# Optimization experiments

Measured on AMD Instinct MI355X. Metric: run time of the kernel, lower is better.

## Reference

```python
import jax, jax.numpy as jnp
import numpy as np

X = 2048      # hidden units per layer
Z = 4         # number of hidden layers
IN = 512      # input_dim
OUT = 256     # output_dim
B = 64        # batch
T = 128       # time steps
KEEP = 0.7    # Bernoulli keep prob y
RES = [0, 0, 1, 2]  # residual_in (first two unused by the branch structure)
NFUN = 5      # number of candidate transfer functions


def setup_inputs() -> dict:
    key = jax.random.key(0)
    ks = jax.random.split(key, 12)
    f32 = jnp.float32
    x = jax.random.normal(ks[0], (B, T, IN), f32)
    W_in = jax.random.normal(ks[1], (X, IN), f32) * jax.random.bernoulli(ks[2], KEEP, (X, IN)).astype(f32)
    b_in = jax.random.normal(ks[3], (X,), f32)
    W_h = jax.random.normal(ks[4], (Z, X, 2 * X), f32)
    # lateral inhibition block: hidden layer 1, second-half columns, zero diagonal
    lat = jax.random.normal(ks[5], (X, X), f32) * (1.0 - jnp.eye(X, dtype=f32))
    W_h = W_h.at[1, :, X:].set(lat)
    W_h = W_h * jax.random.bernoulli(ks[6], KEEP, (Z, X, 2 * X)).astype(f32)
    b_h = jax.random.normal(ks[7], (Z, X), f32)
    W_out = jax.random.normal(ks[8], (OUT, X), f32) * jax.random.bernoulli(ks[9], KEEP, (OUT, X)).astype(f32)
    b_out = jax.random.normal(ks[10], (OUT,), f32)
    act_ids = jax.random.randint(ks[11], (Z + 1, X), 0, NFUN)
    out_act_ids = jax.random.randint(jax.random.fold_in(key, 99), (OUT,), 0, NFUN)
    return dict(x=x, W_in=W_in, b_in=b_in, W_h=W_h, b_h=b_h,
                W_out=W_out, b_out=b_out, act_ids=act_ids, out_act_ids=out_act_ids)


def _rand_act(h, ids):
    # per-column random nonlinearity: ids [D] in {relu, sigmoid, tanh, leaky_relu(0.1), selu}
    stk = jnp.stack([
        jax.nn.relu(h),
        jax.nn.sigmoid(h),
        jnp.tanh(h),
        jnp.where(h >= 0, h, 0.1 * h),
        jax.nn.selu(h),
    ], axis=0)  # [5, B, D]
    oh = jax.nn.one_hot(ids, NFUN, dtype=h.dtype)  # [D, 5]
    return jnp.einsum('fbd,df->bd', stk, oh)


def _l2norm(v, eps=1e-12):
    # torch F.normalize along dim=1
    return v / jnp.maximum(jnp.linalg.norm(v, axis=1, keepdims=True), eps)


def reference(x, W_in, b_in, W_h, b_h, W_out, b_out, act_ids, out_act_ids):
    batch = x.shape[0]

    def step(carry, xt):
        bp, li = carry  # backprojection state, lateral inhibition state
        h0 = _rand_act(xt @ W_in.T + b_in, act_ids[0])
        h1 = _rand_act(jnp.concatenate([h0, bp], axis=-1) @ W_h[0].T + b_h[0], act_ids[1])
        h2 = _rand_act(jnp.concatenate([h1, li], axis=-1) @ W_h[1].T + b_h[1], act_ids[2])
        li_new = _l2norm(h2)
        outs = [h0, h1, h2]
        for i in range(2, Z):
            hin = jnp.concatenate([outs[i], outs[RES[i]]], axis=-1)
            outs.append(_rand_act(hin @ W_h[i].T + b_h[i], act_ids[i + 1]))
        bp_new = _l2norm(outs[-1])
        yt = _rand_act(outs[-1] @ W_out.T + b_out, out_act_ids)
        return (bp_new, li_new), yt

    init = (jnp.zeros((batch, X), x.dtype), jnp.zeros((batch, X), x.dtype))
    _, ys = jax.lax.scan(step, init, jnp.swapaxes(x, 0, 1))  # scan over time
    return jnp.swapaxes(ys, 0, 1)  # [B, T, OUT]
```

## Files before the change

### kernel.cpp

```cpp
#include <hip/hip_runtime.h>
#include <stdint.h>


typedef __bf16 bf16;
typedef __attribute__((ext_vector_type(8))) __bf16 bf16x8;
typedef __attribute__((ext_vector_type(4))) float f32x4;

#define BATCH 64
#define TSTEPS 128
#define INDIM 512
#define XDIM 2048
#define OUTDIM 256
#define SLOTE ((size_t)BATCH * XDIM)
#define NBLOCKS 256
#define GSTRIDE 64

__device__ __forceinline__ float apply_act(float h, int id) {
  switch (id) {
    case 0: return fmaxf(h, 0.0f);
    case 1: return 1.0f / (1.0f + __expf(-h));
    case 2: return tanhf(h);
    case 3: return h >= 0.0f ? h : 0.1f * h;
    default: {
      const float sc = 1.0507009873554805f;
      const float al = 1.6732632423543772f;
      return h > 0.0f ? sc * h : sc * al * (__expf(h) - 1.0f);
    }
  }
}

__device__ __forceinline__ bf16x8 cload(const bf16* p) {
  union { unsigned long long q[2]; bf16x8 v; } u;
  const unsigned long long* qp = (const unsigned long long*)p;
  u.q[0] = __hip_atomic_load(qp, __ATOMIC_RELAXED, __HIP_MEMORY_SCOPE_AGENT);
  u.q[1] = __hip_atomic_load(qp + 1, __ATOMIC_RELAXED, __HIP_MEMORY_SCOPE_AGENT);
  return u.v;
}

__device__ __forceinline__ void cstore8(unsigned long long* p,
                                        unsigned long long v) {
  unsigned long long old = __hip_atomic_exchange(p, v, __ATOMIC_RELAXED,
                                                 __HIP_MEMORY_SCOPE_AGENT);
  asm volatile("" :: "v"(old));
}

__device__ __forceinline__ unsigned long long cload8(
    const unsigned long long* p) {
  return __hip_atomic_load(p, __ATOMIC_RELAXED, __HIP_MEMORY_SCOPE_AGENT);
}

__device__ __forceinline__ void grid_sync2(unsigned* bars, int bid,
                                           unsigned ph) {
  __syncthreads();
  if (threadIdx.x == 0) {
    const int g = bid >> 5;
    unsigned* garr = bars + (size_t)g * GSTRIDE;
    unsigned* gbar = bars + (size_t)8 * GSTRIDE;
    unsigned* rel  = bars + (size_t)(9 + g) * GSTRIDE;
    unsigned old = __hip_atomic_fetch_add(garr, 1u, __ATOMIC_RELAXED,
                                          __HIP_MEMORY_SCOPE_AGENT);
    if (old == 32u * ph - 1u) {
      unsigned gold = __hip_atomic_fetch_add(gbar, 1u, __ATOMIC_RELAXED,
                                             __HIP_MEMORY_SCOPE_AGENT);
      if (gold != 8u * ph - 1u) {
        while (__hip_atomic_load(gbar, __ATOMIC_RELAXED,
                                 __HIP_MEMORY_SCOPE_AGENT) < 8u * ph) {
          __builtin_amdgcn_s_sleep(4);
        }
      }
      __hip_atomic_fetch_add(rel, 1u, __ATOMIC_RELAXED,
                             __HIP_MEMORY_SCOPE_AGENT);
    } else {
      while (__hip_atomic_load(rel, __ATOMIC_RELAXED,
                               __HIP_MEMORY_SCOPE_AGENT) < ph) {
        __builtin_amdgcn_s_sleep(4);
      }
    }
  }
  __syncthreads();
}

template <bool SCALE_A2, bool EMIT_SS, bool PLAIN_A1>
__device__ __forceinline__ void layer_phase(
    const int tid, const int nt, const int kq,
    const bf16* __restrict__ A1, const bf16* __restrict__ A2,
    const bf16x8 (&wf)[2][4], const float* __restrict__ bias,
    const int* __restrict__ acts, const float* __restrict__ ss_in,
    float* __restrict__ ss_out, bf16* __restrict__ outb,
    float* __restrict__ pbuf, unsigned* __restrict__ flags,
    const unsigned ph, float (&red)[8][64][33]) {
  const int lane = tid & 63;
  const int w = tid >> 6;
  const int l15 = lane & 15;
  const int kb8 = (lane >> 4) * 8;
  const int q4 = lane >> 4;

  const bf16* As = (kq >= 2) ? A2 : A1;
  const int koff = (kq & 1) * 1024 + w * 128;
  const bf16* ap = As + (size_t)l15 * 2048 + koff + kb8;

  f32x4 acc[4][2];
  const f32x4 zero = {0.f, 0.f, 0.f, 0.f};
#pragma unroll
  for (int mt = 0; mt < 4; mt++) {
    acc[mt][0] = zero;
    acc[mt][1] = zero;
  }

  const bool plain = PLAIN_A1 && (kq < 2);
#pragma unroll
  for (int ks = 0; ks < 4; ks++) {
#pragma unroll
    for (int mt = 0; mt < 4; mt++) {
      const bf16* aptr = ap + (size_t)mt * 16 * 2048 + ks * 32;
      bf16x8 a = plain ? *(const bf16x8*)aptr : cload(aptr);
      acc[mt][0] = __builtin_amdgcn_mfma_f32_16x16x32_bf16(a, wf[0][ks], acc[mt][0], 0, 0, 0);
      acc[mt][1] = __builtin_amdgcn_mfma_f32_16x16x32_bf16(a, wf[1][ks], acc[mt][1], 0, 0, 0);
    }
  }

#pragma unroll
  for (int mt = 0; mt < 4; mt++)
#pragma unroll
    for (int n2 = 0; n2 < 2; n2++)
#pragma unroll
      for (int r = 0; r < 4; r++)
        red[w][mt * 16 + q4 * 4 + r][n2 * 16 + l15] = acc[mt][n2][r];
  __syncthreads();

  const int row = tid >> 3;
  const int c4 = (tid & 7) * 4;
  float v[4];
#pragma unroll
  for (int j = 0; j < 4; j++) {
    float s = 0.f;
#pragma unroll
    for (int ww = 0; ww < 8; ww++) s += red[ww][row][c4 + j];
    v[j] = s;
  }

  const size_t pidx = ((size_t)row) * XDIM + nt * 32 + c4;
  if (kq != 0) {
    float* pb = pbuf + (size_t)(kq - 1) * BATCH * XDIM + pidx;
    union { float f[2]; unsigned long long u; } pk;
    pk.f[0] = v[0]; pk.f[1] = v[1];
    cstore8((unsigned long long*)pb, pk.u);
    pk.f[0] = v[2]; pk.f[1] = v[3];
    cstore8((unsigned long long*)(pb + 2), pk.u);
    __syncthreads();
    if (tid == 0) {
      __hip_atomic_fetch_add(flags + (size_t)nt * GSTRIDE, 1u,
                             __ATOMIC_RELAXED, __HIP_MEMORY_SCOPE_AGENT);
    }
  } else {
    if (tid == 0) {
      while (__hip_atomic_load(flags + (size_t)nt * GSTRIDE, __ATOMIC_RELAXED,
                               __HIP_MEMORY_SCOPE_AGENT) < 3u * ph) {
        __builtin_amdgcn_s_sleep(2);
      }
    }
    __syncthreads();
    float p1[4], p2[4], p3[4];
#pragma unroll
    for (int h = 0; h < 2; h++) {
      union { unsigned long long u; float f[2]; } u1, u2, u3;
      const unsigned long long* b1 = (const unsigned long long*)(pbuf + pidx) + h;
      u1.u = cload8(b1);
      u2.u = cload8(b1 + (size_t)BATCH * XDIM / 2);
      u3.u = cload8(b1 + (size_t)BATCH * XDIM);
      p1[h * 2] = u1.f[0]; p1[h * 2 + 1] = u1.f[1];
      p2[h * 2] = u2.f[0]; p2[h * 2 + 1] = u2.f[1];
      p3[h * 2] = u3.f[0]; p3[h * 2 + 1] = u3.f[1];
    }
    float scale = 1.0f;
    if (SCALE_A2) {
      float ssv = __hip_atomic_load(ss_in + row, __ATOMIC_RELAXED,
                                    __HIP_MEMORY_SCOPE_AGENT);
      scale = 1.0f / fmaxf(sqrtf(ssv), 1e-12f);
    }
    const int cg = nt * 32 + c4;
    union { bf16 b[4]; unsigned long long u; } hk;
    float ssl = 0.f;
#pragma unroll
    for (int j = 0; j < 4; j++) {
      float lo = v[j] + p1[j];
      float hi = p2[j] + p3[j];
      float pre = (SCALE_A2 ? (lo + scale * hi) : (lo + hi)) + bias[cg + j];
      float av = apply_act(pre, acts[cg + j]);
      hk.b[j] = (bf16)av;
      ssl += av * av;
    }
    if (EMIT_SS) {
      ssl += __shfl_xor(ssl, 1);
      ssl += __shfl_xor(ssl, 2);
      ssl += __shfl_xor(ssl, 4);
      if ((tid & 7) == 0) atomicAdd(ss_out + row, ssl);
    }
    cstore8((unsigned long long*)(outb + (size_t)row * XDIM + cg), hk.u);
  }
}

struct StepParams {
  bf16* h0;
  bf16* extra;
  bf16* h1;
  bf16* h2a;
  bf16* h2b;
  bf16* h3;
  const bf16* whb;
  const float* b_h;
  const int* acts;
  float* ss_li;
  float* ss_bp;
  float* pbuf;
  unsigned* flags;
  unsigned* bar;
};

__global__ __launch_bounds__(512, 2) void step_loop(StepParams p) {
  __shared__ float red[8][64][33];
  const int tid = threadIdx.x;
  const int bid = blockIdx.x;
  const int nt = bid & 63;
  const int kq = bid >> 6;
  const int lane = tid & 63;
  const int w = tid >> 6;
  const int l15 = lane & 15;
  const int kb8 = (lane >> 4) * 8;
  const size_t wstr = (size_t)XDIM * 2 * XDIM;

  const bf16* wb = p.whb + (size_t)(nt * 32 + l15) * 4096 + kq * 1024 +
                   w * 128 + kb8;
  bf16x8 wf0[2][4], wf1[2][4], wf2[2][4], wf3[2][4];
#pragma unroll
  for (int n2 = 0; n2 < 2; n2++) {
#pragma unroll
    for (int ks = 0; ks < 4; ks++) {
      const bf16* q = wb + (size_t)n2 * 16 * 4096 + ks * 32;
      wf0[n2][ks] = *(const bf16x8*)q;
      wf1[n2][ks] = *(const bf16x8*)(q + wstr);
      wf2[n2][ks] = *(const bf16x8*)(q + 2 * wstr);
      wf3[n2][ks] = *(const bf16x8*)(q + 3 * wstr);
    }
  }

  unsigned ph = 0;
  for (int t = 0; t < TSTEPS; t++) {
#pragma unroll
    for (int n2 = 0; n2 < 2; n2++)
#pragma unroll
      for (int ks = 0; ks < 4; ks++) {
        asm volatile("" : "+v"(wf0[n2][ks]), "+v"(wf1[n2][ks]),
                          "+v"(wf2[n2][ks]), "+v"(wf3[n2][ks]));
      }

    const bf16* h4t = (t < 2) ? p.extra + (size_t)t * SLOTE
                              : p.h0 + (size_t)(t - 2) * SLOTE;
    bf16* h4n = (t + 1 < 2) ? p.extra + (size_t)(t + 1) * SLOTE
                            : p.h0 + (size_t)(t - 1) * SLOTE;
    bf16* h2n = (t & 1) ? p.h2b : p.h2a;
    const bf16* h2o = (t & 1) ? p.h2a : p.h2b;

    ++ph;
    layer_phase<true, false, true>(tid, nt, kq, p.h0 + (size_t)t * SLOTE, h4t,
                                   wf0, p.b_h, p.acts + XDIM,
                                   p.ss_bp + t * BATCH, nullptr, p.h1,
                                   p.pbuf, p.flags, ph, red);
    grid_sync2(p.bar, bid, ph);

    ++ph;
    layer_phase<true, true, false>(tid, nt, kq, p.h1, h2o, wf1, p.b_h + XDIM,
                                   p.acts + 2 * XDIM, p.ss_li + t * BATCH,
                                   p.ss_li + (t + 1) * BATCH, h2n,
                                   p.pbuf, p.flags, ph, red);
    grid_sync2(p.bar, bid, ph);

    ++ph;
    layer_phase<false, false, false>(tid, nt, kq, h2n, p.h1, wf2,
                                     p.b_h + 2 * XDIM, p.acts + 3 * XDIM,
                                     nullptr, nullptr, p.h3,
                                     p.pbuf, p.flags, ph, red);
    grid_sync2(p.bar, bid, ph);

    ++ph;
    layer_phase<false, true, false>(tid, nt, kq, p.h3, h2n, wf3,
                                    p.b_h + 3 * XDIM, p.acts + 4 * XDIM,
                                    nullptr, p.ss_bp + (t + 1) * BATCH, h4n,
                                    p.pbuf, p.flags, ph, red);
    grid_sync2(p.bar, bid, ph);
  }
}

__global__ __launch_bounds__(256) void h0_gemm(
    const bf16* __restrict__ A, const bf16* __restrict__ W,
    const float* __restrict__ bias, const int* __restrict__ acts,
    bf16* __restrict__ outp) {
  const int tid = threadIdx.x;
  const int lane = tid & 63;
  const int wv = tid >> 6;
  const int wm = (wv & 1) * 32;
  const int wn = (wv >> 1) * 64;
  const int nblk = blockIdx.x * 128;
  const int mblk = blockIdx.y * 64;
  const int l15 = lane & 15;
  const int kb8 = (lane >> 4) * 8;

  f32x4 acc[2][4];
  const f32x4 zero = {0.f, 0.f, 0.f, 0.f};
#pragma unroll
  for (int i = 0; i < 2; i++)
#pragma unroll
    for (int j = 0; j < 4; j++) acc[i][j] = zero;

  for (int kt = 0; kt < INDIM; kt += 32) {
    bf16x8 a[2], b[4];
#pragma unroll
    for (int mt = 0; mt < 2; mt++) {
      int m = mblk + wm + mt * 16 + l15;
      a[mt] = *(const bf16x8*)(A + (size_t)m * INDIM + kt + kb8);
    }
#pragma unroll
    for (int nt = 0; nt < 4; nt++) {
      int n = nblk + wn + nt * 16 + l15;
      b[nt] = *(const bf16x8*)(W + (size_t)n * INDIM + kt + kb8);
    }
#pragma unroll
    for (int mt = 0; mt < 2; mt++)
#pragma unroll
      for (int nt = 0; nt < 4; nt++)
        acc[mt][nt] = __builtin_amdgcn_mfma_f32_16x16x32_bf16(a[mt], b[nt], acc[mt][nt], 0, 0, 0);
  }

#pragma unroll
  for (int mt = 0; mt < 2; mt++) {
#pragma unroll
    for (int nt = 0; nt < 4; nt++) {
      int n = nblk + wn + nt * 16 + l15;
      float bv = bias[n];
      int aid = acts[n];
#pragma unroll
      for (int rr = 0; rr < 4; rr++) {
        int m = wm + mt * 16 + (lane >> 4) * 4 + rr;
        float v = apply_act(acc[mt][nt][rr] + bv, aid);
        int rowg = mblk + m;
        int bb = rowg >> 7;
        int tt = rowg & 127;
        outp[((size_t)tt * BATCH + bb) * XDIM + n] = (bf16)v;
      }
    }
  }
}

__global__ __launch_bounds__(256) void ybat_gemm(
    const bf16* __restrict__ extra, const bf16* __restrict__ h0,
    const bf16* __restrict__ Wout, const float* __restrict__ bout,
    const int* __restrict__ oact, float* __restrict__ out) {
  const int t = blockIdx.y;
  const int s = t + 1;
  const bf16* A = (s < 2) ? (extra + (size_t)s * SLOTE)
                          : (h0 + (size_t)(s - 2) * SLOTE);
  const int tid = threadIdx.x;
  const int lane = tid & 63;
  const int wv = tid >> 6;
  const int wm = (wv & 1) * 32;
  const int wn = (wv >> 1) * 64;
  const int nblk = blockIdx.x * 128;
  const int l15 = lane & 15;
  const int kb8 = (lane >> 4) * 8;

  f32x4 acc[2][4];
  const f32x4 zero = {0.f, 0.f, 0.f, 0.f};
#pragma unroll
  for (int i = 0; i < 2; i++)
#pragma unroll
    for (int j = 0; j < 4; j++) acc[i][j] = zero;

  for (int kt = 0; kt < XDIM; kt += 32) {
    bf16x8 a[2], b[4];
#pragma unroll
    for (int mt = 0; mt < 2; mt++) {
      int m = wm + mt * 16 + l15;
      a[mt] = *(const bf16x8*)(A + (size_t)m * XDIM + kt + kb8);
    }
#pragma unroll
    for (int nt = 0; nt < 4; nt++) {
      int n = nblk + wn + nt * 16 + l15;
      b[nt] = *(const bf16x8*)(Wout + (size_t)n * XDIM + kt + kb8);
    }
#pragma unroll
    for (int mt = 0; mt < 2; mt++)
#pragma unroll
      for (int nt = 0; nt < 4; nt++)
        acc[mt][nt] = __builtin_amdgcn_mfma_f32_16x16x32_bf16(a[mt], b[nt], acc[mt][nt], 0, 0, 0);
  }

#pragma unroll
  for (int mt = 0; mt < 2; mt++) {
#pragma unroll
    for (int nt = 0; nt < 4; nt++) {
      int n = nblk + wn + nt * 16 + l15;
      float bv = bout[n];
      int aid = oact[n];
#pragma unroll
      for (int rr = 0; rr < 4; rr++) {
        int b = wm + mt * 16 + (lane >> 4) * 4 + rr;
        float v = apply_act(acc[mt][nt][rr] + bv, aid);
        out[((size_t)b * TSTEPS + t) * OUTDIM + n] = v;
      }
    }
  }
}

__global__ __launch_bounds__(256) void cvt_bf16(
    const float* __restrict__ in, bf16* __restrict__ out, int n4) {
  int i = blockIdx.x * 256 + threadIdx.x;
  if (i < n4) {
    float4 v = ((const float4*)in)[i];
    union { bf16 b[4]; unsigned long long u; } pk;
    pk.b[0] = (bf16)v.x;
    pk.b[1] = (bf16)v.y;
    pk.b[2] = (bf16)v.z;
    pk.b[3] = (bf16)v.w;
    ((unsigned long long*)out)[i] = pk.u;
  }
}

__global__ __launch_bounds__(256) void zero32(uint32_t* __restrict__ p, int n) {
  int i = blockIdx.x * 256 + threadIdx.x;
  if (i < n) p[i] = 0u;
}

extern "C" void kernel_launch(void* const* d_in, const int* in_sizes, int n_in,
                              void* d_out, int out_size, void* d_ws, size_t ws_size,
                              hipStream_t stream) {
  const float* x     = (const float*)d_in[0];
  const float* W_in  = (const float*)d_in[1];
  const float* b_in  = (const float*)d_in[2];
  const float* W_h   = (const float*)d_in[3];
  const float* b_h   = (const float*)d_in[4];
  const float* W_out = (const float*)d_in[5];
  const float* b_out = (const float*)d_in[6];
  const int* act_ids = (const int*)d_in[7];
  const int* out_act = (const int*)d_in[8];
  float* out = (float*)d_out;

  char* w = (char*)d_ws;
  bf16* xbf   = (bf16*)w; w += (size_t)BATCH * TSTEPS * INDIM * 2;
  bf16* winb  = (bf16*)w; w += (size_t)XDIM * INDIM * 2;
  bf16* whb   = (bf16*)w; w += (size_t)4 * XDIM * (2 * XDIM) * 2;
  bf16* woutb = (bf16*)w; w += (size_t)OUTDIM * XDIM * 2;
  bf16* h0    = (bf16*)w; w += (size_t)TSTEPS * SLOTE * 2;
  bf16* h1    = (bf16*)w; w += SLOTE * 2;
  bf16* h3    = (bf16*)w; w += SLOTE * 2;
  float* pbuf = (float*)w; w += (size_t)3 * BATCH * XDIM * 4;
  char* zstart = w;
  bf16* extra = (bf16*)w; w += 2 * SLOTE * 2;
  bf16* h2a   = (bf16*)w; w += SLOTE * 2;
  bf16* h2b   = (bf16*)w; w += SLOTE * 2;
  float* ss_li = (float*)w; w += (size_t)(TSTEPS + 1) * BATCH * 4;
  float* ss_bp = (float*)w; w += (size_t)(TSTEPS + 1) * BATCH * 4;
  unsigned* flags = (unsigned*)w; w += (size_t)64 * GSTRIDE * 4;
  unsigned* bar = (unsigned*)w; w += (size_t)32 * GSTRIDE * 4;
  int zero_u32 = (int)((w - zstart) / 4);

  cvt_bf16<<<4096, 256, 0, stream>>>(x, xbf, (BATCH * TSTEPS * INDIM) / 4);
  cvt_bf16<<<1024, 256, 0, stream>>>(W_in, winb, (XDIM * INDIM) / 4);
  cvt_bf16<<<32768, 256, 0, stream>>>(W_h, whb, (4 * XDIM * 2 * XDIM) / 4);
  cvt_bf16<<<512, 256, 0, stream>>>(W_out, woutb, (OUTDIM * XDIM) / 4);
  zero32<<<(zero_u32 + 255) / 256, 256, 0, stream>>>((uint32_t*)zstart, zero_u32);
  h0_gemm<<<dim3(16, 128), 256, 0, stream>>>(xbf, winb, b_in, act_ids, h0);

  StepParams sp;
  sp.h0 = h0;
  sp.extra = extra;
  sp.h1 = h1;
  sp.h2a = h2a;
  sp.h2b = h2b;
  sp.h3 = h3;
  sp.whb = whb;
  sp.b_h = b_h;
  sp.acts = act_ids;
  sp.ss_li = ss_li;
  sp.ss_bp = ss_bp;
  sp.pbuf = pbuf;
  sp.flags = flags;
  sp.bar = bar;
  void* kp[] = {&sp};
  (void)hipLaunchCooperativeKernel((const void*)step_loop, dim3(NBLOCKS),
                                   dim3(512), kp, 0, stream);

  ybat_gemm<<<dim3(2, TSTEPS), 256, 0, stream>>>(
      extra, h0, woutb, b_out, out_act, out);
}
```

Before: 8.846 ms.

## Split K eight ways, double-buffer partials, fold grid barrier into reducer arrival

The persistent step kernel now tiles each layer as 32 column tiles of width 64 times 8 K-slices instead of 64 tiles of width 32 times 4 K-slices. Partial sums go into a parity double-buffered pbuf, so writers in the next phase cannot overwrite data still being read. The separate two-level grid barrier is replaced by a barrier where only the 32 reducer blocks increment the global counter and group leaders release the waiting blocks. This cuts barrier latency per phase but makes each reducer read 7 partials instead of 3, and needs more pbuf memory.

```diff
diff --git a/kernel.cpp b/kernel.cpp
--- a/kernel.cpp
+++ b/kernel.cpp
@@ -12,6 +12,8 @@
 #define XDIM 2048
 #define OUTDIM 256
 #define SLOTE ((size_t)BATCH * XDIM)
+#define SLOTF ((size_t)BATCH * XDIM)
+#define PBPAR (7 * SLOTF)
 #define NBLOCKS 256
 #define GSTRIDE 64
 
@@ -49,24 +51,169 @@
   return __hip_atomic_load(p, __ATOMIC_RELAXED, __HIP_MEMORY_SCOPE_AGENT);
 }
 
-__device__ __forceinline__ void grid_sync2(unsigned* bars, int bid,
-                                           unsigned ph) {
-  __syncthreads();
-  if (threadIdx.x == 0) {
-    const int g = bid >> 5;
-    unsigned* garr = bars + (size_t)g * GSTRIDE;
-    unsigned* gbar = bars + (size_t)8 * GSTRIDE;
-    unsigned* rel  = bars + (size_t)(9 + g) * GSTRIDE;
-    unsigned old = __hip_atomic_fetch_add(garr, 1u, __ATOMIC_RELAXED,
-                                          __HIP_MEMORY_SCOPE_AGENT);
-    if (old == 32u * ph - 1u) {
-      unsigned gold = __hip_atomic_fetch_add(gbar, 1u, __ATOMIC_RELAXED,
-                                             __HIP_MEMORY_SCOPE_AGENT);
-      if (gold != 8u * ph - 1u) {
-        while (__hip_atomic_load(gbar, __ATOMIC_RELAXED,
-                                 __HIP_MEMORY_SCOPE_AGENT) < 8u * ph) {
-          __builtin_amdgcn_s_sleep(4);
+template <bool SCALE_A2, bool EMIT_SS, bool PLAIN_A1>
+__device__ __forceinline__ void layer_phase(
+    const int tid, const int nt, const int kq, const int bid,
+    const bf16* __restrict__ A1, const bf16* __restrict__ A2,
+    const bf16x8 (&wf)[4][2], const float* __restrict__ bias,
+    const int* __restrict__ acts, const float* __restrict__ ss_in,
+    float* __restrict__ ss_out, bf16* __restrict__ outb,
+    float* __restrict__ pbuf, unsigned* __restrict__ flags,
+    unsigned* __restrict__ bars, const unsigned ph,
+    float (&red)[8][64][33]) {
+  const int lane = tid & 63;
+  const int w = tid >> 6;
+  const int l15 = lane & 15;
+  const int kb8 = (lane >> 4) * 8;
+  const int q4 = lane >> 4;
+
+  const bf16* As = (kq >= 4) ? A2 : A1;
+  const int koff = (kq & 3) * 512 + w * 64;
+  const bf16* ap = As + (size_t)l15 * 2048 + koff + kb8;
+
+  f32x4 acc[4][4];
+  const f32x4 zero = {0.f, 0.f, 0.f, 0.f};
+#pragma unroll
+  for (int mt = 0; mt < 4; mt++)
+#pragma unroll
+    for (int ntl = 0; ntl < 4; ntl++) acc[mt][ntl] = zero;
+
+  const bool plain = PLAIN_A1 && (kq < 4);
+#pragma unroll
+  for (int ks = 0; ks < 2; ks++) {
+#pragma unroll
+    for (int mt = 0; mt < 4; mt++) {
+      const bf16* aptr = ap + (size_t)mt * 16 * 2048 + ks * 32;
+      bf16x8 a = plain ? *(const bf16x8*)aptr : cload(aptr);
+#pragma unroll
+      for (int ntl = 0; ntl < 4; ntl++)
+        acc[mt][ntl] = __builtin_amdgcn_mfma_f32_16x16x32_bf16(
+            a, wf[ntl][ks], acc[mt][ntl], 0, 0, 0);
+    }
+  }
+
+  const int row = tid >> 3;
+  const int c4 = (tid & 7) * 4;
+  float v[2][4];
+#pragma unroll
+  for (int h = 0; h < 2; h++) {
+#pragma unroll
+    for (int mt = 0; mt < 4; mt++)
+#pragma unroll
+      for (int j = 0; j < 2; j++)
+#pragma unroll
+        for (int r = 0; r < 4; r++)
+          red[w][mt * 16 + q4 * 4 + r][j * 16 + l15] = acc[mt][2 * h + j][r];
+    __syncthreads();
+#pragma unroll
+    for (int jj = 0; jj < 4; jj++) {
+      float s = 0.f;
+#pragma unroll
+      for (int ww = 0; ww < 8; ww++) s += red[ww][row][c4 + jj];
+      v[h][jj] = s;
+    }
+    __syncthreads();
+  }
+
+  const int cbase = nt * 64;
+  unsigned* gbar = bars + (size_t)8 * GSTRIDE;
+
+  if (kq != 0) {
+    float* pb = pbuf + (size_t)(ph & 1) * PBPAR + (size_t)(kq - 1) * SLOTF +
+                (size_t)row * XDIM + cbase;
+#pragma unroll
+    for (int h = 0; h < 2; h++) {
+      union { float f[2]; unsigned long long u; } pk;
+      float* q = pb + h * 32 + c4;
+      pk.f[0] = v[h][0]; pk.f[1] = v[h][1];
+      cstore8((unsigned long long*)q, pk.u);
+      pk.f[0] = v[h][2]; pk.f[1] = v[h][3];
+      cstore8((unsigned long long*)(q + 2), pk.u);
+    }
+    __syncthreads();
+    if (tid == 0) {
+      __hip_atomic_fetch_add(flags + (size_t)nt * GSTRIDE, 1u,
+                             __ATOMIC_RELAXED, __HIP_MEMORY_SCOPE_AGENT);
+    }
+  } else {
+    if (tid == 0) {
+      while (__hip_atomic_load(flags + (size_t)nt * GSTRIDE, __ATOMIC_RELAXED,
+                               __HIP_MEMORY_SCOPE_AGENT) < 7u * ph) {
+        __builtin_amdgcn_s_sleep(2);
+      }
+    }
+    __syncthreads();
+
+    float lo[2][4], hi[2][4];
+#pragma unroll
+    for (int h = 0; h < 2; h++)
+#pragma unroll
+      for (int j = 0; j < 4; j++) {
+        lo[h][j] = v[h][j];
+        hi[h][j] = 0.f;
+      }
+    const float* pbase = pbuf + (size_t)(ph & 1) * PBPAR +
+                         (size_t)row * XDIM + cbase;
+#pragma unroll
+    for (int kqi = 1; kqi < 8; kqi++) {
+      const float* q = pbase + (size_t)(kqi - 1) * SLOTF;
+#pragma unroll
+      for (int h = 0; h < 2; h++) {
+        union { unsigned long long u; float f[2]; } a, b;
+        a.u = cload8((const unsigned long long*)(q + h * 32 + c4));
+        b.u = cload8((const unsigned long long*)(q + h * 32 + c4 + 2));
+        if (kqi < 4) {
+          lo[h][0] += a.f[0]; lo[h][1] += a.f[1];
+          lo[h][2] += b.f[0]; lo[h][3] += b.f[1];
+        } else {
+          hi[h][0] += a.f[0]; hi[h][1] += a.f[1];
+          hi[h][2] += b.f[0]; hi[h][3] += b.f[1];
         }
+      }
+    }
+
+    float scale = 1.0f;
+    if (SCALE_A2) {
+      float ssv = __hip_atomic_load(ss_in + row, __ATOMIC_RELAXED,
+                                    __HIP_MEMORY_SCOPE_AGENT);
+      scale = 1.0f / fmaxf(sqrtf(ssv), 1e-12f);
+    }
+    float ssl = 0.f;
+#pragma unroll
+    for (int h = 0; h < 2; h++) {
+      union { bf16 b[4]; unsigned long long u; } hk;
+#pragma unroll
+      for (int j = 0; j < 4; j++) {
+        int c = cbase + h * 32 + c4 + j;
+        float pre = lo[h][j] + (SCALE_A2 ? scale * hi[h][j] : hi[h][j]) +
+                    bias[c];
+        float av = apply_act(pre, acts[c]);
+        hk.b[j] = (bf16)av;
+        ssl += av * av;
+      }
+      cstore8((unsigned long long*)(outb + (size_t)row * XDIM + cbase +
+                                    h * 32 + c4),
+              hk.u);
+    }
+    if (EMIT_SS) {
+      ssl += __shfl_xor(ssl, 1);
+      ssl += __shfl_xor(ssl, 2);
+      ssl += __shfl_xor(ssl, 4);
+      if ((tid & 7) == 0) atomicAdd(ss_out + row, ssl);
+    }
+    __syncthreads();
+    if (tid == 0) {
+      __hip_atomic_fetch_add(gbar, 1u, __ATOMIC_RELAXED,
+                             __HIP_MEMORY_SCOPE_AGENT);
+    }
+  }
+
+  if (tid == 0) {
+    unsigned* rel = bars + (size_t)(9 + (bid >> 5)) * GSTRIDE;
+    if ((bid & 31) == 0) {
+      while (__hip_atomic_load(gbar, __ATOMIC_RELAXED,
+                               __HIP_MEMORY_SCOPE_AGENT) < 32u * ph) {
+        __builtin_amdgcn_s_sleep(4);
       }
       __hip_atomic_fetch_add(rel, 1u, __ATOMIC_RELAXED,
                              __HIP_MEMORY_SCOPE_AGENT);
@@ -78,126 +225,6 @@
     }
   }
   __syncthreads();
-}
-
-template <bool SCALE_A2, bool EMIT_SS, bool PLAIN_A1>
-__device__ __forceinline__ void layer_phase(
-    const int tid, const int nt, const int kq,
-    const bf16* __restrict__ A1, const bf16* __restrict__ A2,
-    const bf16x8 (&wf)[2][4], const float* __restrict__ bias,
-    const int* __restrict__ acts, const float* __restrict__ ss_in,
-    float* __restrict__ ss_out, bf16* __restrict__ outb,
-    float* __restrict__ pbuf, unsigned* __restrict__ flags,
-    const unsigned ph, float (&red)[8][64][33]) {
-  const int lane = tid & 63;
-  const int w = tid >> 6;
-  const int l15 = lane & 15;
-  const int kb8 = (lane >> 4) * 8;
-  const int q4 = lane >> 4;
-
-  const bf16* As = (kq >= 2) ? A2 : A1;
-  const int koff = (kq & 1) * 1024 + w * 128;
-  const bf16* ap = As + (size_t)l15 * 2048 + koff + kb8;
-
-  f32x4 acc[4][2];
-  const f32x4 zero = {0.f, 0.f, 0.f, 0.f};
-#pragma unroll
-  for (int mt = 0; mt < 4; mt++) {
-    acc[mt][0] = zero;
-    acc[mt][1] = zero;
-  }
-
-  const bool plain = PLAIN_A1 && (kq < 2);
-#pragma unroll
-  for (int ks = 0; ks < 4; ks++) {
-#pragma unroll
-    for (int mt = 0; mt < 4; mt++) {
-      const bf16* aptr = ap + (size_t)mt * 16 * 2048 + ks * 32;
-      bf16x8 a = plain ? *(const bf16x8*)aptr : cload(aptr);
-      acc[mt][0] = __builtin_amdgcn_mfma_f32_16x16x32_bf16(a, wf[0][ks], acc[mt][0], 0, 0, 0);
-      acc[mt][1] = __builtin_amdgcn_mfma_f32_16x16x32_bf16(a, wf[1][ks], acc[mt][1], 0, 0, 0);
-    }
-  }
-
-#pragma unroll
-  for (int mt = 0; mt < 4; mt++)
-#pragma unroll
-    for (int n2 = 0; n2 < 2; n2++)
-#pragma unroll
-      for (int r = 0; r < 4; r++)
-        red[w][mt * 16 + q4 * 4 + r][n2 * 16 + l15] = acc[mt][n2][r];
-  __syncthreads();
-
-  const int row = tid >> 3;
-  const int c4 = (tid & 7) * 4;
-  float v[4];
-#pragma unroll
-  for (int j = 0; j < 4; j++) {
-    float s = 0.f;
-#pragma unroll
-    for (int ww = 0; ww < 8; ww++) s += red[ww][row][c4 + j];
-    v[j] = s;
-  }
-
-  const size_t pidx = ((size_t)row) * XDIM + nt * 32 + c4;
-  if (kq != 0) {
-    float* pb = pbuf + (size_t)(kq - 1) * BATCH * XDIM + pidx;
-    union { float f[2]; unsigned long long u; } pk;
-    pk.f[0] = v[0]; pk.f[1] = v[1];
-    cstore8((unsigned long long*)pb, pk.u);
-    pk.f[0] = v[2]; pk.f[1] = v[3];
-    cstore8((unsigned long long*)(pb + 2), pk.u);
-    __syncthreads();
-    if (tid == 0) {
-      __hip_atomic_fetch_add(flags + (size_t)nt * GSTRIDE, 1u,
-                             __ATOMIC_RELAXED, __HIP_MEMORY_SCOPE_AGENT);
-    }
-  } else {
-    if (tid == 0) {
-      while (__hip_atomic_load(flags + (size_t)nt * GSTRIDE, __ATOMIC_RELAXED,
-                               __HIP_MEMORY_SCOPE_AGENT) < 3u * ph) {
-        __builtin_amdgcn_s_sleep(2);
-      }
-    }
-    __syncthreads();
-    float p1[4], p2[4], p3[4];
-#pragma unroll
-    for (int h = 0; h < 2; h++) {
-      union { unsigned long long u; float f[2]; } u1, u2, u3;
-      const unsigned long long* b1 = (const unsigned long long*)(pbuf + pidx) + h;
-      u1.u = cload8(b1);
-      u2.u = cload8(b1 + (size_t)BATCH * XDIM / 2);
-      u3.u = cload8(b1 + (size_t)BATCH * XDIM);
-      p1[h * 2] = u1.f[0]; p1[h * 2 + 1] = u1.f[1];
-      p2[h * 2] = u2.f[0]; p2[h * 2 + 1] = u2.f[1];
-      p3[h * 2] = u3.f[0]; p3[h * 2 + 1] = u3.f[1];
-    }
-    float scale = 1.0f;
-    if (SCALE_A2) {
-      float ssv = __hip_atomic_load(ss_in + row, __ATOMIC_RELAXED,
-                                    __HIP_MEMORY_SCOPE_AGENT);
-      scale = 1.0f / fmaxf(sqrtf(ssv), 1e-12f);
-    }
-    const int cg = nt * 32 + c4;
-    union { bf16 b[4]; unsigned long long u; } hk;
-    float ssl = 0.f;
-#pragma unroll
-    for (int j = 0; j < 4; j++) {
-      float lo = v[j] + p1[j];
-      float hi = p2[j] + p3[j];
-      float pre = (SCALE_A2 ? (lo + scale * hi) : (lo + hi)) + bias[cg + j];
-      float av = apply_act(pre, acts[cg + j]);
-      hk.b[j] = (bf16)av;
-      ssl += av * av;
-    }
-    if (EMIT_SS) {
-      ssl += __shfl_xor(ssl, 1);
-      ssl += __shfl_xor(ssl, 2);
-      ssl += __shfl_xor(ssl, 4);
-      if ((tid & 7) == 0) atomicAdd(ss_out + row, ssl);
-    }
-    cstore8((unsigned long long*)(outb + (size_t)row * XDIM + cg), hk.u);
-  }
 }
 
 struct StepParams {
@@ -221,37 +248,37 @@
   __shared__ float red[8][64][33];
   const int tid = threadIdx.x;
   const int bid = blockIdx.x;
-  const int nt = bid & 63;
-  const int kq = bid >> 6;
+  const int nt = bid & 31;
+  const int kq = bid >> 5;
   const int lane = tid & 63;
   const int w = tid >> 6;
   const int l15 = lane & 15;
   const int kb8 = (lane >> 4) * 8;
   const size_t wstr = (size_t)XDIM * 2 * XDIM;
 
-  const bf16* wb = p.whb + (size_t)(nt * 32 + l15) * 4096 + kq * 1024 +
-                   w * 128 + kb8;
-  bf16x8 wf0[2][4], wf1[2][4], wf2[2][4], wf3[2][4];
-#pragma unroll
-  for (int n2 = 0; n2 < 2; n2++) {
-#pragma unroll
-    for (int ks = 0; ks < 4; ks++) {
-      const bf16* q = wb + (size_t)n2 * 16 * 4096 + ks * 32;
-      wf0[n2][ks] = *(const bf16x8*)q;
-      wf1[n2][ks] = *(const bf16x8*)(q + wstr);
-      wf2[n2][ks] = *(const bf16x8*)(q + 2 * wstr);
-      wf3[n2][ks] = *(const bf16x8*)(q + 3 * wstr);
+  const bf16* wb = p.whb + (size_t)(nt * 64 + l15) * 4096 + kq * 512 +
+                   w * 64 + kb8;
+  bf16x8 wf0[4][2], wf1[4][2], wf2[4][2], wf3[4][2];
+#pragma unroll
+  for (int ntl = 0; ntl < 4; ntl++) {
+#pragma unroll
+    for (int ks = 0; ks < 2; ks++) {
+      const bf16* q = wb + (size_t)ntl * 16 * 4096 + ks * 32;
+      wf0[ntl][ks] = *(const bf16x8*)q;
+      wf1[ntl][ks] = *(const bf16x8*)(q + wstr);
+      wf2[ntl][ks] = *(const bf16x8*)(q + 2 * wstr);
+      wf3[ntl][ks] = *(const bf16x8*)(q + 3 * wstr);
     }
   }
 
   unsigned ph = 0;
   for (int t = 0; t < TSTEPS; t++) {
 #pragma unroll
-    for (int n2 = 0; n2 < 2; n2++)
-#pragma unroll
-      for (int ks = 0; ks < 4; ks++) {
-        asm volatile("" : "+v"(wf0[n2][ks]), "+v"(wf1[n2][ks]),
-                          "+v"(wf2[n2][ks]), "+v"(wf3[n2][ks]));
+    for (int ntl = 0; ntl < 4; ntl++)
+#pragma unroll
+      for (int ks = 0; ks < 2; ks++) {
+        asm volatile("" : "+v"(wf0[ntl][ks]), "+v"(wf1[ntl][ks]),
+                          "+v"(wf2[ntl][ks]), "+v"(wf3[ntl][ks]));
       }
 
     const bf16* h4t = (t < 2) ? p.extra + (size_t)t * SLOTE
@@ -262,32 +289,30 @@
     const bf16* h2o = (t & 1) ? p.h2a : p.h2b;
 
     ++ph;
-    layer_phase<true, false, true>(tid, nt, kq, p.h0 + (size_t)t * SLOTE, h4t,
-                                   wf0, p.b_h, p.acts + XDIM,
-                                   p.ss_bp + t * BATCH, nullptr, p.h1,
-                                   p.pbuf, p.flags, ph, red);
-    grid_sync2(p.bar, bid, ph);
+    layer_phase<true, false, true>(tid, nt, kq, bid,
+                                   p.h0 + (size_t)t * SLOTE, h4t, wf0, p.b_h,
+                                   p.acts + XDIM, p.ss_bp + t * BATCH,
+                                   nullptr, p.h1, p.pbuf, p.flags, p.bar, ph,
+                                   red);
 
     ++ph;
-    layer_phase<true, true, false>(tid, nt, kq, p.h1, h2o, wf1, p.b_h + XDIM,
-                                   p.acts + 2 * XDIM, p.ss_li + t * BATCH,
-                                   p.ss_li + (t + 1) * BATCH, h2n,
-                                   p.pbuf, p.flags, ph, red);
-    grid_sync2(p.bar, bid, ph);
+    layer_phase<true, true, false>(tid, nt, kq, bid, p.h1, h2o, wf1,
+                                   p.b_h + XDIM, p.acts + 2 * XDIM,
+                                   p.ss_li + t * BATCH,
+                                   p.ss_li + (t + 1) * BATCH, h2n, p.pbuf,
+                                   p.flags, p.bar, ph, red);
 
     ++ph;
-    layer_phase<false, false, false>(tid, nt, kq, h2n, p.h1, wf2,
+    layer_phase<false, false, false>(tid, nt, kq, bid, h2n, p.h1, wf2,
                                      p.b_h + 2 * XDIM, p.acts + 3 * XDIM,
-                                     nullptr, nullptr, p.h3,
-                                     p.pbuf, p.flags, ph, red);
-    grid_sync2(p.bar, bid, ph);
+                                     nullptr, nullptr, p.h3, p.pbuf, p.flags,
+                                     p.bar, ph, red);
 
     ++ph;
-    layer_phase<false, true, false>(tid, nt, kq, p.h3, h2n, wf3,
+    layer_phase<false, true, false>(tid, nt, kq, bid, p.h3, h2n, wf3,
                                     p.b_h + 3 * XDIM, p.acts + 4 * XDIM,
                                     nullptr, p.ss_bp + (t + 1) * BATCH, h4n,
-                                    p.pbuf, p.flags, ph, red);
-    grid_sync2(p.bar, bid, ph);
+                                    p.pbuf, p.flags, p.bar, ph, red);
   }
 }
 
@@ -452,7 +477,7 @@
   bf16* h0    = (bf16*)w; w += (size_t)TSTEPS * SLOTE * 2;
   bf16* h1    = (bf16*)w; w += SLOTE * 2;
   bf16* h3    = (bf16*)w; w += SLOTE * 2;
-  float* pbuf = (float*)w; w += (size_t)3 * BATCH * XDIM * 4;
+  float* pbuf = (float*)w; w += (size_t)2 * PBPAR * 4;
   char* zstart = w;
   bf16* extra = (bf16*)w; w += 2 * SLOTE * 2;
   bf16* h2a   = (bf16*)w; w += SLOTE * 2;
```

Result: slower. 14.42 ms (+63.0%).

## Replace full grid barrier with producer-count release and double-buffer partials

Applied to the files above, without the earlier changes.

The all-block hierarchical barrier after each layer phase is replaced by a scheme where only the 64 finalizing blocks (kq==0) increment a done counter. A per-group leader waits for all 64 and then releases its group. The split-K partial buffer is double-buffered by phase parity so that writers of the next phase cannot overwrite partials still being read. Sleep intervals are shortened. This cuts the number of atomics on the barrier's critical path, at the cost of extra workspace and subtler memory-ordering assumptions.

```diff
diff --git a/kernel.cpp b/kernel.cpp
--- a/kernel.cpp
+++ b/kernel.cpp
@@ -14,6 +14,7 @@
 #define SLOTE ((size_t)BATCH * XDIM)
 #define NBLOCKS 256
 #define GSTRIDE 64
+#define PBPAR ((size_t)3 * BATCH * XDIM)
 
 __device__ __forceinline__ float apply_act(float h, int id) {
   switch (id) {
@@ -49,31 +50,22 @@
   return __hip_atomic_load(p, __ATOMIC_RELAXED, __HIP_MEMORY_SCOPE_AGENT);
 }
 
-__device__ __forceinline__ void grid_sync2(unsigned* bars, int bid,
+__device__ __forceinline__ void phase_wait(unsigned* bars, int bid,
                                            unsigned ph) {
-  __syncthreads();
   if (threadIdx.x == 0) {
-    const int g = bid >> 5;
-    unsigned* garr = bars + (size_t)g * GSTRIDE;
-    unsigned* gbar = bars + (size_t)8 * GSTRIDE;
-    unsigned* rel  = bars + (size_t)(9 + g) * GSTRIDE;
-    unsigned old = __hip_atomic_fetch_add(garr, 1u, __ATOMIC_RELAXED,
-                                          __HIP_MEMORY_SCOPE_AGENT);
-    if (old == 32u * ph - 1u) {
-      unsigned gold = __hip_atomic_fetch_add(gbar, 1u, __ATOMIC_RELAXED,
-                                             __HIP_MEMORY_SCOPE_AGENT);
-      if (gold != 8u * ph - 1u) {
-        while (__hip_atomic_load(gbar, __ATOMIC_RELAXED,
-                                 __HIP_MEMORY_SCOPE_AGENT) < 8u * ph) {
-          __builtin_amdgcn_s_sleep(4);
-        }
+    unsigned* done = bars + (size_t)8 * GSTRIDE;
+    unsigned* rel = bars + (size_t)(9 + (bid >> 5)) * GSTRIDE;
+    if ((bid & 31) == 0) {
+      while (__hip_atomic_load(done, __ATOMIC_RELAXED,
+                               __HIP_MEMORY_SCOPE_AGENT) < 64u * ph) {
+        __builtin_amdgcn_s_sleep(2);
       }
       __hip_atomic_fetch_add(rel, 1u, __ATOMIC_RELAXED,
                              __HIP_MEMORY_SCOPE_AGENT);
     } else {
       while (__hip_atomic_load(rel, __ATOMIC_RELAXED,
                                __HIP_MEMORY_SCOPE_AGENT) < ph) {
-        __builtin_amdgcn_s_sleep(4);
+        __builtin_amdgcn_s_sleep(2);
       }
     }
   }
@@ -88,7 +80,8 @@
     const int* __restrict__ acts, const float* __restrict__ ss_in,
     float* __restrict__ ss_out, bf16* __restrict__ outb,
     float* __restrict__ pbuf, unsigned* __restrict__ flags,
-    const unsigned ph, float (&red)[8][64][33]) {
+    unsigned* __restrict__ bars, const unsigned ph,
+    float (&red)[8][64][33]) {
   const int lane = tid & 63;
   const int w = tid >> 6;
   const int l15 = lane & 15;
@@ -139,9 +132,10 @@
     v[j] = s;
   }
 
+  float* pbase = pbuf + (size_t)(ph & 1) * PBPAR;
   const size_t pidx = ((size_t)row) * XDIM + nt * 32 + c4;
   if (kq != 0) {
-    float* pb = pbuf + (size_t)(kq - 1) * BATCH * XDIM + pidx;
+    float* pb = pbase + (size_t)(kq - 1) * BATCH * XDIM + pidx;
     union { float f[2]; unsigned long long u; } pk;
     pk.f[0] = v[0]; pk.f[1] = v[1];
     cstore8((unsigned long long*)pb, pk.u);
@@ -156,7 +150,7 @@
     if (tid == 0) {
       while (__hip_atomic_load(flags + (size_t)nt * GSTRIDE, __ATOMIC_RELAXED,
                                __HIP_MEMORY_SCOPE_AGENT) < 3u * ph) {
-        __builtin_amdgcn_s_sleep(2);
+        __builtin_amdgcn_s_sleep(1);
       }
     }
     __syncthreads();
@@ -164,7 +158,8 @@
 #pragma unroll
     for (int h = 0; h < 2; h++) {
       union { unsigned long long u; float f[2]; } u1, u2, u3;
-      const unsigned long long* b1 = (const unsigned long long*)(pbuf + pidx) + h;
+      const unsigned long long* b1 =
+          (const unsigned long long*)(pbase + pidx) + h;
       u1.u = cload8(b1);
       u2.u = cload8(b1 + (size_t)BATCH * XDIM / 2);
       u3.u = cload8(b1 + (size_t)BATCH * XDIM);
@@ -197,6 +192,11 @@
       if ((tid & 7) == 0) atomicAdd(ss_out + row, ssl);
     }
     cstore8((unsigned long long*)(outb + (size_t)row * XDIM + cg), hk.u);
+    __syncthreads();
+    if (tid == 0) {
+      __hip_atomic_fetch_add(bars + (size_t)8 * GSTRIDE, 1u, __ATOMIC_RELAXED,
+                             __HIP_MEMORY_SCOPE_AGENT);
+    }
   }
 }
 
@@ -265,29 +265,29 @@
     layer_phase<true, false, true>(tid, nt, kq, p.h0 + (size_t)t * SLOTE, h4t,
                                    wf0, p.b_h, p.acts + XDIM,
                                    p.ss_bp + t * BATCH, nullptr, p.h1,
-                                   p.pbuf, p.flags, ph, red);
-    grid_sync2(p.bar, bid, ph);
+                                   p.pbuf, p.flags, p.bar, ph, red);
+    phase_wait(p.bar, bid, ph);
 
     ++ph;
     layer_phase<true, true, false>(tid, nt, kq, p.h1, h2o, wf1, p.b_h + XDIM,
                                    p.acts + 2 * XDIM, p.ss_li + t * BATCH,
                                    p.ss_li + (t + 1) * BATCH, h2n,
-                                   p.pbuf, p.flags, ph, red);
-    grid_sync2(p.bar, bid, ph);
+                                   p.pbuf, p.flags, p.bar, ph, red);
+    phase_wait(p.bar, bid, ph);
 
     ++ph;
     layer_phase<false, false, false>(tid, nt, kq, h2n, p.h1, wf2,
                                      p.b_h + 2 * XDIM, p.acts + 3 * XDIM,
                                      nullptr, nullptr, p.h3,
-                                     p.pbuf, p.flags, ph, red);
-    grid_sync2(p.bar, bid, ph);
+                                     p.pbuf, p.flags, p.bar, ph, red);
+    phase_wait(p.bar, bid, ph);
 
     ++ph;
     layer_phase<false, true, false>(tid, nt, kq, p.h3, h2n, wf3,
                                     p.b_h + 3 * XDIM, p.acts + 4 * XDIM,
                                     nullptr, p.ss_bp + (t + 1) * BATCH, h4n,
-                                    p.pbuf, p.flags, ph, red);
-    grid_sync2(p.bar, bid, ph);
+                                    p.pbuf, p.flags, p.bar, ph, red);
+    phase_wait(p.bar, bid, ph);
   }
 }
 
@@ -452,7 +452,7 @@
   bf16* h0    = (bf16*)w; w += (size_t)TSTEPS * SLOTE * 2;
   bf16* h1    = (bf16*)w; w += SLOTE * 2;
   bf16* h3    = (bf16*)w; w += SLOTE * 2;
-  float* pbuf = (float*)w; w += (size_t)3 * BATCH * XDIM * 4;
+  float* pbuf = (float*)w; w += (size_t)2 * PBPAR * 4;
   char* zstart = w;
   bf16* extra = (bf16*)w; w += 2 * SLOTE * 2;
   bf16* h2a   = (bf16*)w; w += SLOTE * 2;
```

Result: faster. 8.597 ms (-2.8%).
